# Optimization experiments

Hardware: AMD Instinct MI355X
Metric: run time of the kernel (lower is better)

## Reference

```python
import jax, jax.numpy as jnp
import numpy as np

N_QUBITS = 7
DEPTH = 2
DIM = 2 ** N_QUBITS  # 128
BATCH = 262144

# Qiskit little-endian convention: statevector index bit q = (idx >> q) & 1.
_idx = np.arange(DIM)
_bits = (_idx[:, None] >> np.arange(N_QUBITS)) & 1            # (DIM, N_QUBITS)
# CZ on all adjacent pairs (q, q+1): sign = (-1)^sum(bit_q * bit_{q+1})
_cz_parity = np.sum(_bits[:, :-1] * _bits[:, 1:], axis=1) % 2
CZ_PHASE = jnp.asarray(1.0 - 2.0 * _cz_parity, dtype=jnp.float32)   # (DIM,)
# Z_i expectation signs: <Z_i> = sum_idx p(idx) * (1 - 2*bit_i)
Z_SIGNS = jnp.asarray(1.0 - 2.0 * _bits, dtype=jnp.float32)         # (DIM, N_QUBITS)


def _apply_ry(state, q, theta_q):
    # state: (B, DIM) real amplitudes; RY is real so state stays real.
    lo = 2 ** q
    hi = DIM // (2 * lo)
    s = state.reshape(-1, hi, 2, lo)
    half = theta_q * 0.5
    c, sn = jnp.cos(half), jnp.sin(half)
    a0, a1 = s[:, :, 0, :], s[:, :, 1, :]
    out = jnp.stack([c * a0 - sn * a1, sn * a0 + c * a1], axis=2)
    return out.reshape(-1, DIM)


def setup_inputs() -> dict:
    key = jax.random.key(0)
    k1, k2 = jax.random.split(key)
    embed = jax.random.normal(k1, (BATCH, DIM), dtype=jnp.float32)
    theta = jax.random.normal(k2, (DEPTH * N_QUBITS,), dtype=jnp.float32) * 0.1
    return {"embed": embed, "theta": theta}


def reference(embed, theta):
    # Amplitude encoding: L2-normalize each row.
    state = embed / jnp.linalg.norm(embed, axis=1, keepdims=True)
    for d in range(DEPTH):
        for q in range(N_QUBITS):
            state = _apply_ry(state, q, theta[d * N_QUBITS + q])
        state = state * CZ_PHASE[None, :]
    probs = state * state                  # (B, DIM)
    return probs @ Z_SIGNS                 # (B, N_QUBITS)
```

## Files before the change

### kernel.cpp

```cpp
#include <hip/hip_runtime.h>

#define NQ   7
#define DIM  128

__global__ __launch_bounds__(64, 2)
void qnat_kernel(const float* __restrict__ embed,
                 const float* __restrict__ theta,
                 float* __restrict__ out)
{
    __shared__ float lds[64 * 33];
    const int lane = threadIdx.x;
    const size_t rowBase = (size_t)blockIdx.x * 64;
    const float4* __restrict__ g4 =
        reinterpret_cast<const float4*>(embed + rowBase * DIM);
    const int gr = lane >> 3;
    const int gq = lane & 7;

    float st[DIM];

    float4 buf[8];
#pragma unroll
    for (int j = 0; j < 8; ++j)
        buf[j] = g4[(j * 8 + gr) * 32 + gq];

#pragma unroll
    for (int c = 0; c < 4; ++c) {
        float4 nxt[8];
        if (c < 3) {
#pragma unroll
            for (int j = 0; j < 8; ++j)
                nxt[j] = g4[(j * 8 + gr) * 32 + (c + 1) * 8 + gq];
        }
#pragma unroll
        for (int j = 0; j < 8; ++j) {
            const int base = (j * 8 + gr) * 33 + gq * 4;
            lds[base + 0] = buf[j].x;
            lds[base + 1] = buf[j].y;
            lds[base + 2] = buf[j].z;
            lds[base + 3] = buf[j].w;
        }
        __syncthreads();
#pragma unroll
        for (int j = 0; j < 8; ++j) {
            const int base = lane * 33 + j * 4;
            st[c * 32 + j * 4 + 0] = lds[base + 0];
            st[c * 32 + j * 4 + 1] = lds[base + 1];
            st[c * 32 + j * 4 + 2] = lds[base + 2];
            st[c * 32 + j * 4 + 3] = lds[base + 3];
        }
        __syncthreads();
        if (c < 3) {
#pragma unroll
            for (int j = 0; j < 8; ++j) buf[j] = nxt[j];
        }
    }

    float ss = 0.f;
#pragma unroll
    for (int i = 0; i < DIM; ++i) ss = fmaf(st[i], st[i], ss);
    const float inv = __builtin_amdgcn_rsqf(ss);
#pragma unroll
    for (int i = 0; i < DIM; ++i) st[i] *= inv;

#pragma clang loop unroll(disable)
    for (int d = 0; d < 2; ++d) {
#pragma unroll
        for (int q = 0; q < NQ; ++q) {
            const float half = 0.5f * theta[d * NQ + q];
            const float c_ = __cosf(half);
            const float s_ = __sinf(half);
            const int lo = 1 << q;
#pragma unroll
            for (int p = 0; p < 64; ++p) {
                const int i0 = ((p >> q) << (q + 1)) | (p & (lo - 1));
                const int i1 = i0 | lo;
                const float a0 = st[i0], a1 = st[i1];
                st[i0] = fmaf(c_, a0, -s_ * a1);
                st[i1] = fmaf(s_, a0,  c_ * a1);
            }
        }
#pragma unroll
        for (int i = 0; i < DIM; ++i) {
            int par = 0;
#pragma unroll
            for (int j = 0; j < NQ - 1; ++j)
                par ^= ((i >> j) & 1) & ((i >> (j + 1)) & 1);
            if (par) st[i] = -st[i];
        }
    }

#pragma unroll
    for (int i = 0; i < DIM; ++i) st[i] *= st[i];

    float o[NQ];
#pragma unroll
    for (int k = 0; k < NQ; ++k) {
        const int n = DIM >> (k + 1);
        float acc = 0.f;
#pragma unroll
        for (int i = 0; i < 64; ++i) {
            if (i < n) {
                const float a = st[2 * i], b = st[2 * i + 1];
                acc += a - b;
                st[i] = a + b;
            }
        }
        o[k] = acc;
    }

    __syncthreads();
#pragma unroll
    for (int k = 0; k < NQ; ++k) lds[lane * NQ + k] = o[k];
    __syncthreads();
    float* __restrict__ ob = out + rowBase * NQ;
#pragma unroll
    for (int k = 0; k < NQ; ++k) ob[k * 64 + lane] = lds[k * 64 + lane];
}

extern "C" void kernel_launch(void* const* d_in, const int* in_sizes, int n_in,
                              void* d_out, int out_size, void* d_ws, size_t ws_size,
                              hipStream_t stream)
{
    const float* embed = (const float*)d_in[0];
    const float* theta = (const float*)d_in[1];
    float* out = (float*)d_out;
    const int batch = in_sizes[0] / DIM;
    dim3 grid(batch / 64), block(64);
    hipLaunchKernelGGL(qnat_kernel, grid, block, 0, stream, embed, theta, out);
}
```

Before: 199.3 us.

## Load rows directly per thread, defer normalization to output, fully unroll depth

Each thread now reads its own row with 32 direct float4 loads, replacing the LDS-transposed, double-buffered cooperative load and its barriers. The L2 normalization is moved from the 128 amplitudes to the 7 outputs: the circuit is linear and orthogonal, so scaling the final expectations by 1/||x||^2 gives the same result. The depth loop is now fully unrolled and the occupancy hint is raised to 3 blocks per CU. The risk is uncoalesced strided global loads, since each lane reads a separate 512-byte row, plus higher register pressure from the unrolled depth loop under a tighter register budget.

```diff
diff --git a/kernel.cpp b/kernel.cpp
--- a/kernel.cpp
+++ b/kernel.cpp
@@ -3,66 +3,31 @@
 #define NQ   7
 #define DIM  128
 
-__global__ __launch_bounds__(64, 2)
+__global__ __launch_bounds__(64, 3)
 void qnat_kernel(const float* __restrict__ embed,
                  const float* __restrict__ theta,
                  float* __restrict__ out)
 {
-    __shared__ float lds[64 * 33];
     const int lane = threadIdx.x;
-    const size_t rowBase = (size_t)blockIdx.x * 64;
+    const size_t row = (size_t)blockIdx.x * 64 + lane;
     const float4* __restrict__ g4 =
-        reinterpret_cast<const float4*>(embed + rowBase * DIM);
-    const int gr = lane >> 3;
-    const int gq = lane & 7;
+        reinterpret_cast<const float4*>(embed) + row * 32;
 
     float st[DIM];
-
-    float4 buf[8];
 #pragma unroll
-    for (int j = 0; j < 8; ++j)
-        buf[j] = g4[(j * 8 + gr) * 32 + gq];
-
-#pragma unroll
-    for (int c = 0; c < 4; ++c) {
-        float4 nxt[8];
-        if (c < 3) {
-#pragma unroll
-            for (int j = 0; j < 8; ++j)
-                nxt[j] = g4[(j * 8 + gr) * 32 + (c + 1) * 8 + gq];
-        }
-#pragma unroll
-        for (int j = 0; j < 8; ++j) {
-            const int base = (j * 8 + gr) * 33 + gq * 4;
-            lds[base + 0] = buf[j].x;
-            lds[base + 1] = buf[j].y;
-            lds[base + 2] = buf[j].z;
-            lds[base + 3] = buf[j].w;
-        }
-        __syncthreads();
-#pragma unroll
-        for (int j = 0; j < 8; ++j) {
-            const int base = lane * 33 + j * 4;
-            st[c * 32 + j * 4 + 0] = lds[base + 0];
-            st[c * 32 + j * 4 + 1] = lds[base + 1];
-            st[c * 32 + j * 4 + 2] = lds[base + 2];
-            st[c * 32 + j * 4 + 3] = lds[base + 3];
-        }
-        __syncthreads();
-        if (c < 3) {
-#pragma unroll
-            for (int j = 0; j < 8; ++j) buf[j] = nxt[j];
-        }
+    for (int j = 0; j < 32; ++j) {
+        const float4 v = g4[j];
+        st[4 * j + 0] = v.x;
+        st[4 * j + 1] = v.y;
+        st[4 * j + 2] = v.z;
+        st[4 * j + 3] = v.w;
     }
 
     float ss = 0.f;
 #pragma unroll
     for (int i = 0; i < DIM; ++i) ss = fmaf(st[i], st[i], ss);
-    const float inv = __builtin_amdgcn_rsqf(ss);
+
 #pragma unroll
-    for (int i = 0; i < DIM; ++i) st[i] *= inv;
-
-#pragma clang loop unroll(disable)
     for (int d = 0; d < 2; ++d) {
 #pragma unroll
         for (int q = 0; q < NQ; ++q) {
@@ -108,11 +73,15 @@
         o[k] = acc;
     }
 
-    __syncthreads();
+    const float invss = __builtin_amdgcn_rcpf(ss);
+#pragma unroll
+    for (int k = 0; k < NQ; ++k) o[k] *= invss;
+
+    __shared__ float lds[64 * NQ];
 #pragma unroll
     for (int k = 0; k < NQ; ++k) lds[lane * NQ + k] = o[k];
     __syncthreads();
-    float* __restrict__ ob = out + rowBase * NQ;
+    float* __restrict__ ob = out + (size_t)blockIdx.x * (64 * NQ);
 #pragma unroll
     for (int k = 0; k < NQ; ++k) ob[k * 64 + lane] = lds[k * 64 + lane];
 }
```

After: 379.9 us. 1.91x slower.
